# Kernel tuning notes

Hardware: AMD Instinct MI355X
Metric: run time of the kernel (lower is better)

Reference implementation:

```python
import jax, jax.numpy as jnp
import numpy as np

D_MODEL = 1024
N_HEADS = 16
D_K = D_MODEL // N_HEADS
WINDOW = 512
ROPE_BASE = 10000.0


def _apply_rope(x):
    # x: [B, H, S, D] ; torchtune-style interleaved-pair RoPE
    S, D = x.shape[2], x.shape[3]
    half = D // 2
    inv_freq = 1.0 / (ROPE_BASE ** (jnp.arange(half, dtype=jnp.float32) / half))
    ang = jnp.arange(S, dtype=jnp.float32)[:, None] * inv_freq[None, :]  # [S, half]
    cos = jnp.cos(ang).astype(x.dtype)  # [S, half]
    sin = jnp.sin(ang).astype(x.dtype)
    x_even = x[..., ::2]   # [B,H,S,half]
    x_odd = x[..., 1::2]
    out_even = x_even * cos - x_odd * sin
    out_odd = x_odd * cos + x_even * sin
    return jnp.stack([out_even, out_odd], axis=-1).reshape(x.shape)


def setup_inputs() -> dict:
    key = jax.random.key(0)
    k1, k2, k3 = jax.random.split(key, 3)
    B, S = 2, 2048
    x = jax.random.normal(k1, (B, S, D_MODEL), dtype=jnp.float32)
    # store weights pre-transposed so y = x @ w (same math as nn.Linear)
    w_qkv = jax.random.normal(k2, (D_MODEL, 3 * D_MODEL), dtype=jnp.float32) * (D_MODEL ** -0.5)
    w_o = jax.random.normal(k3, (D_MODEL, D_MODEL), dtype=jnp.float32) * (D_MODEL ** -0.5)
    return {"x": x, "w_qkv": w_qkv, "w_o": w_o}


def reference(x, w_qkv, w_o):
    B, S, _ = x.shape
    qkv = (x @ w_qkv).reshape(B, S, 3, N_HEADS, D_K)
    qkv = jnp.transpose(qkv, (2, 0, 3, 1, 4))  # [3, B, H, S, Dk]
    q, k, v = qkv[0], qkv[1], qkv[2]
    q = _apply_rope(q)
    k = _apply_rope(k)
    # causal sliding-window mask: token i attends to j in [i - WINDOW, i]
    i = jnp.arange(S)[:, None]
    j = jnp.arange(S)[None, :]
    allowed = (j <= i) & (j >= i - WINDOW)
    bias = jnp.where(allowed, 0.0, -jnp.inf).astype(x.dtype)  # [S, S]
    scores = jnp.einsum('bhqd,bhkd->bhqk', q, k) * (D_K ** -0.5) + bias
    attn = jax.nn.softmax(scores, axis=-1)
    out = jnp.einsum('bhqk,bhkd->bhqd', attn, v)  # [B,H,S,Dk]
    out = jnp.transpose(out, (0, 2, 1, 3)).reshape(B, S, D_MODEL)
    return out @ w_o
```

## Files before the change

kernel.cpp:

```cpp
#include <hip/hip_runtime.h>
#include <hip/hip_bf16.h>
#include <math.h>

typedef __bf16 bhalf;
typedef __bf16 bhalf8 __attribute__((ext_vector_type(8)));
typedef float floatx4 __attribute__((ext_vector_type(4)));
typedef _Float16 fh;
typedef _Float16 half4 __attribute__((ext_vector_type(4)));

#define MFMA_BF16(A, B, C) __builtin_amdgcn_mfma_f32_16x16x32_bf16((A), (B), (C), 0, 0, 0)
#define MFMA_F16_K16(A, B, C) __builtin_amdgcn_mfma_f32_16x16x16f16((A), (B), (C), 0, 0, 0)

__device__ inline unsigned short bfb(float f) {
  union { bhalf h; unsigned short u; } c;
  c.h = (bhalf)f;
  return c.u;
}
__device__ inline unsigned short fhb(float f) {
  union { fh h; unsigned short u; } c;
  c.h = (fh)f;
  return c.u;
}

__device__ inline void gload_lds16(const void* g, void* l) {
  typedef const __attribute__((address_space(1))) unsigned int GU;
  typedef __attribute__((address_space(3))) unsigned int LU;
  __builtin_amdgcn_global_load_lds((GU*)g, (LU*)l, 16, 0, 0);
}

__global__ __launch_bounds__(256) void prep_kernel(const float* __restrict__ x,
                                                   const float* __restrict__ wqkv,
                                                   const float* __restrict__ wo,
                                                   bhalf* __restrict__ x_bf,
                                                   bhalf* __restrict__ wqkvT,
                                                   bhalf* __restrict__ woT) {
  __shared__ float tile[32][33];
  const int bx = blockIdx.x;
  if (bx < 2048) {
    int i = (bx * 256 + threadIdx.x) * 8;
    floatx4 v0 = *(const floatx4*)(x + i);
    floatx4 v1 = *(const floatx4*)(x + i + 4);
    bhalf8 o;
    o[0] = (bhalf)v0[0]; o[1] = (bhalf)v0[1]; o[2] = (bhalf)v0[2]; o[3] = (bhalf)v0[3];
    o[4] = (bhalf)v1[0]; o[5] = (bhalf)v1[1]; o[6] = (bhalf)v1[2]; o[7] = (bhalf)v1[3];
    *(bhalf8*)(x_bf + i) = o;
    return;
  }
  const float* in;
  bhalf* out;
  int C, cx, ry;
  if (bx < 5120) {
    int idx = bx - 2048;
    in = wqkv; out = wqkvT; C = 3072;
    cx = idx % 96; ry = idx / 96;
  } else {
    int idx = bx - 5120;
    in = wo; out = woT; C = 1024;
    cx = idx & 31; ry = idx >> 5;
  }
  const int R = 1024;
  int c0 = cx * 32, r0 = ry * 32;
  int tx = threadIdx.x & 31, ty = threadIdx.x >> 5;
#pragma unroll
  for (int i = 0; i < 32; i += 8)
    tile[ty + i][tx] = in[(size_t)(r0 + ty + i) * C + c0 + tx];
  __syncthreads();
#pragma unroll
  for (int i = 0; i < 32; i += 8)
    out[(size_t)(c0 + ty + i) * R + r0 + tx] = (bhalf)tile[tx][ty + i];
}

template <int EPI, int TN>
__global__ __launch_bounds__(256, 2) void gemm_bt_kernel(
    const bhalf* __restrict__ A, const bhalf* __restrict__ BT, float* __restrict__ Cout,
    bhalf* __restrict__ qb, bhalf* __restrict__ kb, fh* __restrict__ vb,
    int M, int N, int K) {
  constexpr int NT = TN / 32;
  __shared__ __attribute__((aligned(16))) bhalf As[2][128 * 64];
  __shared__ __attribute__((aligned(16))) bhalf Bs[2][TN * 64];
  const int tid = threadIdx.x;
  const int lane = tid & 63;
  const int w = tid >> 6, wr = w >> 1, wc = w & 1;
  const int m0 = blockIdx.y * 128, n0 = blockIdx.x * TN;
  const int l15 = lane & 15, lhi = lane >> 4;

  floatx4 acc[4][NT];
#pragma unroll
  for (int i = 0; i < 4; ++i)
#pragma unroll
    for (int j = 0; j < NT; ++j) acc[i][j] = (floatx4){0.f, 0.f, 0.f, 0.f};

  const int srow16 = lane >> 2;
  const int scg = (lane & 3) ^ ((lane >> 3) & 3);
  const bhalf* aP0 = A + (size_t)(m0 + 32 * w + srow16) * K + scg * 8;
  const bhalf* aP1 = aP0 + (size_t)16 * K;
  const bhalf* bP0 = BT + (size_t)(n0 + ((TN == 128) ? 32 * w : 16 * w) + srow16) * K + scg * 8;
  const bhalf* bP1 = bP0 + (size_t)16 * K;

  const int fro = (l15 * 4 + (lhi ^ ((l15 >> 1) & 3))) * 8;

  auto stage = [&](int k0, int s) {
    gload_lds16(aP0 + k0, &As[s][(2 * w) * 512]);
    gload_lds16(aP1 + k0, &As[s][(2 * w + 1) * 512]);
    gload_lds16(aP0 + k0 + 32, &As[s][4096 + (2 * w) * 512]);
    gload_lds16(aP1 + k0 + 32, &As[s][4096 + (2 * w + 1) * 512]);
    if constexpr (TN == 128) {
      gload_lds16(bP0 + k0, &Bs[s][(2 * w) * 512]);
      gload_lds16(bP1 + k0, &Bs[s][(2 * w + 1) * 512]);
      gload_lds16(bP0 + k0 + 32, &Bs[s][TN * 32 + (2 * w) * 512]);
      gload_lds16(bP1 + k0 + 32, &Bs[s][TN * 32 + (2 * w + 1) * 512]);
    } else {
      gload_lds16(bP0 + k0, &Bs[s][w * 512]);
      gload_lds16(bP0 + k0 + 32, &Bs[s][TN * 32 + w * 512]);
    }
  };
  auto compute = [&](int s) {
#pragma unroll
    for (int kh = 0; kh < 2; ++kh) {
      bhalf8 af[4], bf[NT];
#pragma unroll
      for (int mt = 0; mt < 4; ++mt)
        af[mt] = *(const bhalf8*)&As[s][kh * 4096 + (wr * 4 + mt) * 512 + fro];
#pragma unroll
      for (int nt = 0; nt < NT; ++nt)
        bf[nt] = *(const bhalf8*)&Bs[s][kh * TN * 32 + (wc * NT + nt) * 512 + fro];
#pragma unroll
      for (int mt = 0; mt < 4; ++mt)
#pragma unroll
        for (int nt = 0; nt < NT; ++nt)
          acc[mt][nt] = MFMA_BF16(af[mt], bf[nt], acc[mt][nt]);
    }
  };

  stage(0, 0);
  int buf = 0;
  for (int k0 = 0; k0 < K; k0 += 64) {
    __syncthreads();
    if (k0 + 64 < K) stage(k0 + 64, buf ^ 1);
    compute(buf);
    buf ^= 1;
  }

  if constexpr (EPI == 0) {
#pragma unroll
    for (int mt = 0; mt < 4; ++mt)
#pragma unroll
      for (int nt = 0; nt < NT; ++nt)
#pragma unroll
        for (int r = 0; r < 4; ++r) {
          int mg = m0 + wr * 64 + mt * 16 + lhi * 4 + r;
          int ng = n0 + wc * (TN / 2) + nt * 16 + l15;
          Cout[(size_t)mg * N + ng] = acc[mt][nt][r];
        }
  } else {
    const int sel = n0 >> 10;
    if (sel == 2) {
#pragma unroll
      for (int mt = 0; mt < 4; ++mt) {
        int mg = m0 + wr * 64 + mt * 16 + lhi * 4;
        int b = mg >> 11, s0 = mg & 2047;
#pragma unroll
        for (int nt = 0; nt < NT; ++nt) {
          int ng = n0 + wc * (TN / 2) + nt * 16 + l15;
          int h = (ng & 1023) >> 6, d = ng & 63;
          union { unsigned short u[4]; uint2 v2; } pk;
#pragma unroll
          for (int r = 0; r < 4; ++r) pk.u[r] = fhb(acc[mt][nt][r]);
          *(uint2*)&vb[((size_t)((b << 4) + h) * 64 + d) * 2048 + s0] = pk.v2;
        }
      }
    } else {
      bhalf* dst = sel ? kb : qb;
#pragma unroll
      for (int nt = 0; nt < NT; ++nt) {
        int ng = n0 + wc * (TN / 2) + nt * 16 + l15;
        int h = (ng & 1023) >> 6, d = ng & 63;
        float inv = exp2f((float)(d >> 1) * -0.4152410118609203f);
#pragma unroll
        for (int mt = 0; mt < 4; ++mt) {
          int mg = m0 + wr * 64 + mt * 16 + lhi * 4;
          int b = mg >> 11, s0 = mg & 2047;
#pragma unroll
          for (int r = 0; r < 4; ++r) {
            float val = acc[mt][nt][r];
            float partner = __shfl_xor(val, 1, 64);
            if (!(l15 & 1)) {
              float ang = (float)(s0 + r) * inv;
              float sn = __sinf(ang), cs = __cosf(ang);
              float oe = cs * val - sn * partner;
              float oo = cs * partner + sn * val;
              unsigned int u = bfb(oe) | ((unsigned int)bfb(oo) << 16);
              *(unsigned int*)&dst[((size_t)((b << 4) + h) * 2048 + (s0 + r)) * 64 + d] = u;
            }
          }
        }
      }
    }
  }
}

__global__ __launch_bounds__(256, 3) void attn_kernel(const bhalf* __restrict__ qg,
                                                      const bhalf* __restrict__ kg,
                                                      const fh* __restrict__ vt,
                                                      bhalf* __restrict__ attn_out) {
  __shared__ __attribute__((aligned(16))) bhalf Ks[2][8 * 512];
  __shared__ __attribute__((aligned(16))) fh Vs[2][16 * 256];

  const int bh = blockIdx.x;
  const int qt2 = blockIdx.y;
  const int tid = threadIdx.x, lane = tid & 63, w = tid >> 6;
  const int l15 = lane & 15, quad = lane >> 4;
  const int q0 = qt2 * 128;
  const int qtile0 = qt2 * 2;
  const size_t base = (size_t)bh * 2048 * 64;
  const size_t vbase = (size_t)bh * 64 * 2048;

  bhalf8 qa[2][2];
#pragma unroll
  for (int h = 0; h < 2; ++h) {
    const bhalf* qp = qg + base + (size_t)(q0 + h * 64 + w * 16 + l15) * 64 + quad * 8;
    bhalf8 t0 = *(const bhalf8*)qp;
    bhalf8 t1 = *(const bhalf8*)(qp + 32);
#pragma unroll
    for (int j = 0; j < 8; ++j) {
      qa[h][0][j] = (bhalf)((float)t0[j] * 0.18033688f);
      qa[h][1][j] = (bhalf)((float)t1[j] * 0.18033688f);
    }
  }

  const int kOff = (w * 16 + (lane >> 2)) * 64 + (lane & 3) * 8;
  const int vfb0 = 4 * w + (lane >> 5), vfb1 = 4 * w + 2 + (lane >> 5);
  const int vOff0 = ((vfb0 & 3) * 16 + ((lane & 31) >> 1)) * 2048 + w * 16 + (lane & 1) * 8;
  const int vOff1 = ((vfb1 & 3) * 16 + ((lane & 31) >> 1)) * 2048 + w * 16 + (lane & 1) * 8;

  floatx4 O[2][4];
#pragma unroll
  for (int h = 0; h < 2; ++h)
#pragma unroll
    for (int dt = 0; dt < 4; ++dt) O[h][dt] = (floatx4){0.f, 0.f, 0.f, 0.f};
  float lsum[2] = {0.f, 0.f};

  auto stage = [&](int kt, int buf) {
    const bhalf* kp = kg + base + (size_t)(kt * 64) * 64 + kOff;
    gload_lds16(kp, &Ks[buf][(2 * w) * 512]);
    gload_lds16(kp + 32, &Ks[buf][(2 * w + 1) * 512]);
    const fh* vp = vt + vbase + kt * 64;
    gload_lds16(vp + vOff0, &Vs[buf][(2 * w) * 512]);
    gload_lds16(vp + vOff1, &Vs[buf][(2 * w + 1) * 512]);
  };

  auto proc = [&](int buf, int kt, int h) {
    const int diag = qtile0 + h;
    if (kt > diag || kt < diag - 8) return;
    const int iG = q0 + h * 64 + w * 16 + l15;
    floatx4 sf[4];
#pragma unroll
    for (int nt = 0; nt < 4; ++nt) {
      bhalf8 k0 = *(const bhalf8*)&Ks[buf][(nt * 2) * 512 + (l15 * 4 + quad) * 8];
      bhalf8 k1 = *(const bhalf8*)&Ks[buf][(nt * 2 + 1) * 512 + (l15 * 4 + quad) * 8];
      floatx4 s = (floatx4){0.f, 0.f, 0.f, 0.f};
      s = MFMA_BF16(k0, qa[h][0], s);
      s = MFMA_BF16(k1, qa[h][1], s);
      sf[nt] = s;
    }
    if (kt == diag) {
#pragma unroll
      for (int nt = 0; nt < 4; ++nt) {
        int jb = kt * 64 + nt * 16 + quad * 4;
#pragma unroll
        for (int r = 0; r < 4; ++r)
          if (jb + r > iG) sf[nt][r] = -1e30f;
      }
    } else if (kt == diag - 8) {
#pragma unroll
      for (int nt = 0; nt < 4; ++nt) {
        int jb = kt * 64 + nt * 16 + quad * 4;
#pragma unroll
        for (int r = 0; r < 4; ++r)
          if (jb + r + 512 < iG) sf[nt][r] = -1e30f;
      }
    }
#pragma unroll
    for (int nt = 0; nt < 4; ++nt) {
      half4 pf;
#pragma unroll
      for (int r = 0; r < 4; ++r) {
        float p = exp2f(sf[nt][r]);
        lsum[h] += p;
        pf[r] = (fh)p;
      }
#pragma unroll
      for (int dt = 0; dt < 4; ++dt) {
        half4 vf = *(const half4*)&Vs[buf][(nt * 4 + dt) * 256 + (l15 * 4 + quad) * 4];
        O[h][dt] = MFMA_F16_K16(vf, pf, O[h][dt]);
      }
    }
  };

  int ktstart = qtile0 - 8;
  if (ktstart < 0) ktstart = 0;
  const int ktend = qtile0 + 1;
  for (int kt = ktstart; kt <= ktend; kt += 2) {
    const bool two = (kt + 1 <= ktend);
    __syncthreads();
    stage(kt, 0);
    if (two) stage(kt + 1, 1);
    __syncthreads();
    proc(0, kt, 0);
    proc(0, kt, 1);
    if (two) {
      proc(1, kt + 1, 0);
      proc(1, kt + 1, 1);
    }
  }

  const int b = bh >> 4, hh = bh & 15;
#pragma unroll
  for (int h = 0; h < 2; ++h) {
    float t = lsum[h];
    t += __shfl_xor(t, 16, 64);
    t += __shfl_xor(t, 32, 64);
    const float inv = 1.f / t;
    const int s = q0 + h * 64 + w * 16 + l15;
#pragma unroll
    for (int dt = 0; dt < 4; ++dt) {
      union { unsigned short u[4]; uint2 v2; } pk;
#pragma unroll
      for (int r = 0; r < 4; ++r) pk.u[r] = bfb(O[h][dt][r] * inv);
      *(uint2*)&attn_out[(size_t)(b * 2048 + s) * 1024 + hh * 64 + dt * 16 + quad * 4] = pk.v2;
    }
  }
}

extern "C" void kernel_launch(void* const* d_in, const int* in_sizes, int n_in,
                              void* d_out, int out_size, void* d_ws, size_t ws_size,
                              hipStream_t stream) {
  (void)in_sizes; (void)n_in; (void)out_size; (void)ws_size;
  const float* x = (const float*)d_in[0];
  const float* w_qkv = (const float*)d_in[1];
  const float* w_o = (const float*)d_in[2];
  float* out = (float*)d_out;
  char* ws = (char*)d_ws;

  bhalf* x_bf  = (bhalf*)(ws);
  bhalf* wqkvT = (bhalf*)(ws + ((size_t)8 << 20));
  bhalf* woT   = (bhalf*)(ws + ((size_t)14 << 20));
  bhalf* qb    = (bhalf*)(ws + ((size_t)16 << 20));
  bhalf* kb    = (bhalf*)(ws + ((size_t)24 << 20));
  fh*    vb    = (fh*)(ws + ((size_t)32 << 20));
  bhalf* attn  = (bhalf*)(ws + ((size_t)40 << 20));

  prep_kernel<<<6144, 256, 0, stream>>>(x, w_qkv, w_o, x_bf, wqkvT, woT);
  gemm_bt_kernel<1, 128><<<dim3(24, 32), 256, 0, stream>>>(x_bf, wqkvT, nullptr, qb, kb, vb,
                                                           4096, 3072, 1024);
  attn_kernel<<<dim3(32, 16), 256, 0, stream>>>(qb, kb, vb, attn);
  gemm_bt_kernel<0, 64><<<dim3(16, 32), 256, 0, stream>>>(attn, woT, out, nullptr, nullptr,
                                                          nullptr, 4096, 1024, 1024);
}
```

Baseline: 169.4 us.

## Halve GEMM k-tile, fold q scale into RoPE epilogue, drop attn tail branch

The GEMM k-step drops from 64 to 32, halving shared memory per stage. This may allow more resident blocks, but it doubles the number of barriers and loop iterations. The softmax scale (including log2e) for q now moves into the QKV GEMM's RoPE epilogue, so the attention kernel loads q directly without a per-element rescale. The attention loop also always processes key tiles in pairs and drops the conditional, relying on ktstart and ktend giving an even count.

```diff
diff --git a/kernel.cpp b/kernel.cpp
--- a/kernel.cpp
+++ b/kernel.cpp
@@ -76,8 +76,8 @@
     bhalf* __restrict__ qb, bhalf* __restrict__ kb, fh* __restrict__ vb,
     int M, int N, int K) {
   constexpr int NT = TN / 32;
-  __shared__ __attribute__((aligned(16))) bhalf As[2][128 * 64];
-  __shared__ __attribute__((aligned(16))) bhalf Bs[2][TN * 64];
+  __shared__ __attribute__((aligned(16))) bhalf As[2][128 * 32];
+  __shared__ __attribute__((aligned(16))) bhalf Bs[2][TN * 32];
   const int tid = threadIdx.x;
   const int lane = tid & 63;
   const int w = tid >> 6, wr = w >> 1, wc = w & 1;
@@ -102,41 +102,33 @@
   auto stage = [&](int k0, int s) {
     gload_lds16(aP0 + k0, &As[s][(2 * w) * 512]);
     gload_lds16(aP1 + k0, &As[s][(2 * w + 1) * 512]);
-    gload_lds16(aP0 + k0 + 32, &As[s][4096 + (2 * w) * 512]);
-    gload_lds16(aP1 + k0 + 32, &As[s][4096 + (2 * w + 1) * 512]);
     if constexpr (TN == 128) {
       gload_lds16(bP0 + k0, &Bs[s][(2 * w) * 512]);
       gload_lds16(bP1 + k0, &Bs[s][(2 * w + 1) * 512]);
-      gload_lds16(bP0 + k0 + 32, &Bs[s][TN * 32 + (2 * w) * 512]);
-      gload_lds16(bP1 + k0 + 32, &Bs[s][TN * 32 + (2 * w + 1) * 512]);
     } else {
       gload_lds16(bP0 + k0, &Bs[s][w * 512]);
-      gload_lds16(bP0 + k0 + 32, &Bs[s][TN * 32 + w * 512]);
     }
   };
   auto compute = [&](int s) {
-#pragma unroll
-    for (int kh = 0; kh < 2; ++kh) {
-      bhalf8 af[4], bf[NT];
-#pragma unroll
-      for (int mt = 0; mt < 4; ++mt)
-        af[mt] = *(const bhalf8*)&As[s][kh * 4096 + (wr * 4 + mt) * 512 + fro];
+    bhalf8 af[4], bf[NT];
+#pragma unroll
+    for (int mt = 0; mt < 4; ++mt)
+      af[mt] = *(const bhalf8*)&As[s][(wr * 4 + mt) * 512 + fro];
+#pragma unroll
+    for (int nt = 0; nt < NT; ++nt)
+      bf[nt] = *(const bhalf8*)&Bs[s][(wc * NT + nt) * 512 + fro];
+#pragma unroll
+    for (int mt = 0; mt < 4; ++mt)
 #pragma unroll
       for (int nt = 0; nt < NT; ++nt)
-        bf[nt] = *(const bhalf8*)&Bs[s][kh * TN * 32 + (wc * NT + nt) * 512 + fro];
-#pragma unroll
-      for (int mt = 0; mt < 4; ++mt)
-#pragma unroll
-        for (int nt = 0; nt < NT; ++nt)
-          acc[mt][nt] = MFMA_BF16(af[mt], bf[nt], acc[mt][nt]);
-    }
+        acc[mt][nt] = MFMA_BF16(af[mt], bf[nt], acc[mt][nt]);
   };
 
   stage(0, 0);
   int buf = 0;
-  for (int k0 = 0; k0 < K; k0 += 64) {
+  for (int k0 = 0; k0 < K; k0 += 32) {
     __syncthreads();
-    if (k0 + 64 < K) stage(k0 + 64, buf ^ 1);
+    if (k0 + 32 < K) stage(k0 + 32, buf ^ 1);
     compute(buf);
     buf ^= 1;
   }
@@ -171,6 +163,7 @@
       }
     } else {
       bhalf* dst = sel ? kb : qb;
+      const float post = sel ? 1.0f : 0.18033688f;
 #pragma unroll
       for (int nt = 0; nt < NT; ++nt) {
         int ng = n0 + wc * (TN / 2) + nt * 16 + l15;
@@ -187,8 +180,8 @@
             if (!(l15 & 1)) {
               float ang = (float)(s0 + r) * inv;
               float sn = __sinf(ang), cs = __cosf(ang);
-              float oe = cs * val - sn * partner;
-              float oo = cs * partner + sn * val;
+              float oe = (cs * val - sn * partner) * post;
+              float oo = (cs * partner + sn * val) * post;
               unsigned int u = bfb(oe) | ((unsigned int)bfb(oo) << 16);
               *(unsigned int*)&dst[((size_t)((b << 4) + h) * 2048 + (s0 + r)) * 64 + d] = u;
             }
@@ -219,13 +212,8 @@
 #pragma unroll
   for (int h = 0; h < 2; ++h) {
     const bhalf* qp = qg + base + (size_t)(q0 + h * 64 + w * 16 + l15) * 64 + quad * 8;
-    bhalf8 t0 = *(const bhalf8*)qp;
-    bhalf8 t1 = *(const bhalf8*)(qp + 32);
-#pragma unroll
-    for (int j = 0; j < 8; ++j) {
-      qa[h][0][j] = (bhalf)((float)t0[j] * 0.18033688f);
-      qa[h][1][j] = (bhalf)((float)t1[j] * 0.18033688f);
-    }
+    qa[h][0] = *(const bhalf8*)qp;
+    qa[h][1] = *(const bhalf8*)(qp + 32);
   }
 
   const int kOff = (w * 16 + (lane >> 2)) * 64 + (lane & 3) * 8;
@@ -301,17 +289,14 @@
   if (ktstart < 0) ktstart = 0;
   const int ktend = qtile0 + 1;
   for (int kt = ktstart; kt <= ktend; kt += 2) {
-    const bool two = (kt + 1 <= ktend);
     __syncthreads();
     stage(kt, 0);
-    if (two) stage(kt + 1, 1);
+    stage(kt + 1, 1);
     __syncthreads();
     proc(0, kt, 0);
     proc(0, kt, 1);
-    if (two) {
-      proc(1, kt + 1, 0);
-      proc(1, kt + 1, 1);
-    }
+    proc(1, kt + 1, 0);
+    proc(1, kt + 1, 1);
   }
 
   const int b = bh >> 4, hh = bh & 15;
```

Measured after the change: 166.6 us. Within noise of the previous version (-1.6%).
